# Optimization experiments

Measured on AMD Instinct MI355X. Metric: run time of the kernel, lower is better.

## Reference

```python
import jax, jax.numpy as jnp
import numpy as np
from jax import lax

CROP = 4
DATA_RANGE = 255.0
KSIZE = 11


def _box_filter(x):
    # x: [B,1,H,W]; 11x11 uniform kernel, padding 5 (SAME), single channel
    k = jnp.ones((1, 1, KSIZE, KSIZE), dtype=x.dtype) / (KSIZE * KSIZE)
    return lax.conv_general_dilated(
        x, k, window_strides=(1, 1), padding=[(5, 5), (5, 5)],
        dimension_numbers=("NCHW", "OIHW", "NCHW"))


def setup_inputs() -> dict:
    key = jax.random.key(0)
    k1, k2 = jax.random.split(key)
    img1 = jax.random.uniform(k1, (16, 3, 512, 512), dtype=jnp.float32) * DATA_RANGE
    img2 = jax.random.uniform(k2, (16, 3, 512, 512), dtype=jnp.float32) * DATA_RANGE
    return {"img1": img1, "img2": img2}


def reference(img1, img2):
    # only_test_y_channel: take channel 0
    x1 = img1[:, 0:1, :, :]
    x2 = img2[:, 0:1, :, :]
    # crop_border = 4
    x1 = x1[:, :, CROP:-CROP, CROP:-CROP].astype(jnp.float32)
    x2 = x2[:, :, CROP:-CROP, CROP:-CROP].astype(jnp.float32)

    C1 = (0.01 * DATA_RANGE) ** 2
    C2 = (0.03 * DATA_RANGE) ** 2

    mu1 = _box_filter(x1)
    mu2 = _box_filter(x2)
    mu1_sq = mu1 * mu1
    mu2_sq = mu2 * mu2
    mu1_mu2 = mu1 * mu2
    sigma1_sq = _box_filter(x1 * x1) - mu1_sq
    sigma2_sq = _box_filter(x2 * x2) - mu2_sq
    sigma12 = _box_filter(x1 * x2) - mu1_mu2

    ssim_map = ((2 * mu1_mu2 + C1) * (2 * sigma12 + C2)) / (
        (mu1_sq + mu2_sq + C1) * (sigma1_sq + sigma2_sq + C2))
    return jnp.mean(ssim_map)
```

## Files before the change

### kernel.cpp

```cpp
#include <hip/hip_runtime.h>

#define CROPPX 4
#define H 504
#define W 504
#define IMG 512
#define NB 16
#define NCH 3
#define KS 11
#define RAD 5
#define TW 64
#define STRIP (TW + 2*RAD)
#define RPS 18
#define NSEG 28
#define NXT 8
#define ROWS (RPS + 2*RAD)
#define CHUNK 7

__global__ __launch_bounds__(64) void ssim_main(const float* __restrict__ img1,
                                                const float* __restrict__ img2,
                                                float* __restrict__ partial) {
    const int tid = threadIdx.x;
    const int gx0 = blockIdx.x * TW;
    const int y0  = blockIdx.y * RPS;
    const int b   = blockIdx.z;

    __shared__ float2 strip[ROWS][STRIP];

    const float* p1 = img1 + (size_t)(b * NCH) * IMG * IMG + (size_t)CROPPX * IMG + CROPPX;
    const float* p2 = img2 + (size_t)(b * NCH) * IMG * IMG + (size_t)CROPPX * IMG + CROPPX;

    const int c0 = gx0 - RAD + tid;
    const int c1 = c0 + 64;
    const bool lane2 = tid < (STRIP - 64);
    const bool c0ok = (unsigned)c0 < (unsigned)W;
    const bool c1ok = lane2 && ((unsigned)c1 < (unsigned)W);

    #pragma unroll
    for (int rc = 0; rc < ROWS / CHUNK; ++rc) {
        float a0[CHUNK], b0[CHUNK], a1[CHUNK], b1[CHUNK];
        #pragma unroll
        for (int j = 0; j < CHUNK; ++j) {
            const int r = y0 - RAD + rc * CHUNK + j;
            a0[j] = 0.f; b0[j] = 0.f; a1[j] = 0.f; b1[j] = 0.f;
            if ((unsigned)r < (unsigned)H) {
                const size_t ro = (size_t)r * IMG;
                if (c0ok) { a0[j] = p1[ro + c0]; b0[j] = p2[ro + c0]; }
                if (c1ok) { a1[j] = p1[ro + c1]; b1[j] = p2[ro + c1]; }
            }
        }
        #pragma unroll
        for (int j = 0; j < CHUNK; ++j) {
            const int r = rc * CHUNK + j;
            strip[r][tid] = make_float2(a0[j], b0[j]);
            if (lane2) strip[r][64 + tid] = make_float2(a1[j], b1[j]);
        }
    }
    __syncthreads();

    float r1[KS], r2[KS], r11[KS], r22[KS], r12[KS];
    #pragma unroll
    for (int j = 0; j < KS; ++j) { r1[j]=0.f; r2[j]=0.f; r11[j]=0.f; r22[j]=0.f; r12[j]=0.f; }

    float vs1 = 0.f, vs2 = 0.f, vs11 = 0.f, vs22 = 0.f, vs12 = 0.f;
    float ssum = 0.f;
    const float C1 = 6.5025f, C2 = 58.5225f;
    const float inv121 = 1.0f / 121.0f;
    const bool colValid = (gx0 + tid) < W;

    for (int base = 0; base < ROWS; base += KS) {
        #pragma unroll
        for (int j = 0; j < KS; ++j) {
            const int iter = base + j;
            if (iter >= ROWS) break;

            float h1 = 0.f, h2 = 0.f, h11 = 0.f, h22 = 0.f, h12 = 0.f;
            #pragma unroll
            for (int dx = 0; dx < KS; ++dx) {
                const float2 ab = strip[iter][tid + dx];
                h1 += ab.x;
                h2 += ab.y;
                h11 = fmaf(ab.x, ab.x, h11);
                h22 = fmaf(ab.y, ab.y, h22);
                h12 = fmaf(ab.x, ab.y, h12);
            }

            vs1  += h1  - r1[j];  r1[j]  = h1;
            vs2  += h2  - r2[j];  r2[j]  = h2;
            vs11 += h11 - r11[j]; r11[j] = h11;
            vs22 += h22 - r22[j]; r22[j] = h22;
            vs12 += h12 - r12[j]; r12[j] = h12;

            if (iter >= 2 * RAD && colValid) {
                const float mu1 = vs1 * inv121;
                const float mu2 = vs2 * inv121;
                const float mu1s = mu1 * mu1;
                const float mu2s = mu2 * mu2;
                const float m12  = mu1 * mu2;
                const float s1  = fmaf(vs11, inv121, -mu1s);
                const float s2  = fmaf(vs22, inv121, -mu2s);
                const float s12 = fmaf(vs12, inv121, -m12);
                const float num = (2.0f * m12 + C1) * (2.0f * s12 + C2);
                const float den = (mu1s + mu2s + C1) * (s1 + s2 + C2);
                ssum = fmaf(num, __builtin_amdgcn_rcpf(den), ssum);
            }
        }
    }

    for (int off = 32; off > 0; off >>= 1)
        ssum += __shfl_down(ssum, off);
    if (tid == 0) {
        const int bidx = (blockIdx.z * gridDim.y + blockIdx.y) * gridDim.x + blockIdx.x;
        partial[bidx] = ssum;
    }
}

__global__ __launch_bounds__(256) void ssim_final(const float* __restrict__ partial,
                                                  int n, float* __restrict__ out) {
    __shared__ double sh[256];
    double s = 0.0;
    for (int i = threadIdx.x; i < n; i += 256) s += (double)partial[i];
    sh[threadIdx.x] = s;
    __syncthreads();
    for (int stride = 128; stride > 0; stride >>= 1) {
        if (threadIdx.x < stride) sh[threadIdx.x] += sh[threadIdx.x + stride];
        __syncthreads();
    }
    if (threadIdx.x == 0)
        out[0] = (float)(sh[0] / ((double)NB * (double)H * (double)W));
}

extern "C" void kernel_launch(void* const* d_in, const int* in_sizes, int n_in,
                              void* d_out, int out_size, void* d_ws, size_t ws_size,
                              hipStream_t stream) {
    const float* img1 = (const float*)d_in[0];
    const float* img2 = (const float*)d_in[1];
    float* out = (float*)d_out;
    float* partial = (float*)d_ws;

    dim3 grid(NXT, NSEG, NB);
    ssim_main<<<grid, 64, 0, stream>>>(img1, img2, partial);
    ssim_final<<<1, 256, 0, stream>>>(partial, NXT * NSEG * NB, out);
}
```

Measured before the change: 143.7 us.

## Stream rows through an 11-row LDS ring buffer with register prefetch

The kernel no longer stages the whole row strip in shared memory behind a block barrier. It keeps an 11-row ring buffer in LDS and prefetches input rows two ahead in registers, using a wave barrier in place of __syncthreads. This overlaps global loads with compute and cuts LDS use per block. Rows per segment also go from 18 to 21, which reduces the number of blocks and the redundant halo loads. The loop is now fully unrolled over 31 rows, which may raise register pressure and code size, and the clamped unconditional loads add a few instructions.

```diff
diff --git a/kernel.cpp b/kernel.cpp
--- a/kernel.cpp
+++ b/kernel.cpp
@@ -10,11 +10,10 @@
 #define RAD 5
 #define TW 64
 #define STRIP (TW + 2*RAD)
-#define RPS 18
-#define NSEG 28
+#define RPS 21
+#define NSEG 24
 #define NXT 8
-#define ROWS (RPS + 2*RAD)
-#define CHUNK 7
+#define TOTAL (RPS + 2*RAD)
 
 __global__ __launch_bounds__(64) void ssim_main(const float* __restrict__ img1,
                                                 const float* __restrict__ img2,
@@ -24,38 +23,18 @@
     const int y0  = blockIdx.y * RPS;
     const int b   = blockIdx.z;
 
-    __shared__ float2 strip[ROWS][STRIP];
+    __shared__ float2 buf[KS][STRIP];
 
     const float* p1 = img1 + (size_t)(b * NCH) * IMG * IMG + (size_t)CROPPX * IMG + CROPPX;
     const float* p2 = img2 + (size_t)(b * NCH) * IMG * IMG + (size_t)CROPPX * IMG + CROPPX;
 
-    const int c0 = gx0 - RAD + tid;
-    const int c1 = c0 + 64;
+    const int  c0   = gx0 - RAD + tid;
+    const int  c0c  = min(max(c0, 0), W - 1);
+    const bool c0ok = (unsigned)c0 < (unsigned)W;
+    const int  c1   = c0 + 64;
+    const int  c1c  = min(c1, W - 1);
+    const bool c1ok = (unsigned)c1 < (unsigned)W;
     const bool lane2 = tid < (STRIP - 64);
-    const bool c0ok = (unsigned)c0 < (unsigned)W;
-    const bool c1ok = lane2 && ((unsigned)c1 < (unsigned)W);
-
-    #pragma unroll
-    for (int rc = 0; rc < ROWS / CHUNK; ++rc) {
-        float a0[CHUNK], b0[CHUNK], a1[CHUNK], b1[CHUNK];
-        #pragma unroll
-        for (int j = 0; j < CHUNK; ++j) {
-            const int r = y0 - RAD + rc * CHUNK + j;
-            a0[j] = 0.f; b0[j] = 0.f; a1[j] = 0.f; b1[j] = 0.f;
-            if ((unsigned)r < (unsigned)H) {
-                const size_t ro = (size_t)r * IMG;
-                if (c0ok) { a0[j] = p1[ro + c0]; b0[j] = p2[ro + c0]; }
-                if (c1ok) { a1[j] = p1[ro + c1]; b1[j] = p2[ro + c1]; }
-            }
-        }
-        #pragma unroll
-        for (int j = 0; j < CHUNK; ++j) {
-            const int r = rc * CHUNK + j;
-            strip[r][tid] = make_float2(a0[j], b0[j]);
-            if (lane2) strip[r][64 + tid] = make_float2(a1[j], b1[j]);
-        }
-    }
-    __syncthreads();
 
     float r1[KS], r2[KS], r11[KS], r22[KS], r12[KS];
     #pragma unroll
@@ -67,44 +46,70 @@
     const float inv121 = 1.0f / 121.0f;
     const bool colValid = (gx0 + tid) < W;
 
-    for (int base = 0; base < ROWS; base += KS) {
+    float sa0[2], sb0[2], sa1[2], sb1[2];
+
+    #define LOAD_ROW(slot, rowIdx)                                            \
+    {                                                                         \
+        const int r_  = (rowIdx);                                             \
+        const int rc_ = min(max(r_, 0), H - 1);                               \
+        const bool rok_ = (unsigned)r_ < (unsigned)H;                         \
+        const size_t ro_ = (size_t)rc_ * IMG;                                 \
+        const float ta0_ = p1[ro_ + c0c], tb0_ = p2[ro_ + c0c];               \
+        sa0[slot] = (rok_ && c0ok) ? ta0_ : 0.f;                              \
+        sb0[slot] = (rok_ && c0ok) ? tb0_ : 0.f;                              \
+        float ta1_ = 0.f, tb1_ = 0.f;                                         \
+        if (lane2) { ta1_ = p1[ro_ + c1c]; tb1_ = p2[ro_ + c1c]; }            \
+        sa1[slot] = (rok_ && c1ok) ? ta1_ : 0.f;                              \
+        sb1[slot] = (rok_ && c1ok) ? tb1_ : 0.f;                              \
+    }
+
+    LOAD_ROW(0, y0 - RAD)
+    LOAD_ROW(1, y0 - RAD + 1)
+
+    #pragma unroll
+    for (int iter = 0; iter < TOTAL; ++iter) {
+        const int slot = iter % KS;
+        const int par  = iter & 1;
+
+        buf[slot][tid] = make_float2(sa0[par], sb0[par]);
+        if (lane2) buf[slot][64 + tid] = make_float2(sa1[par], sb1[par]);
+
+        if (iter + 2 < TOTAL) LOAD_ROW(par, y0 - RAD + iter + 2)
+
+        __builtin_amdgcn_wave_barrier();
+
+        float h1 = 0.f, h2 = 0.f, h11 = 0.f, h22 = 0.f, h12 = 0.f;
         #pragma unroll
-        for (int j = 0; j < KS; ++j) {
-            const int iter = base + j;
-            if (iter >= ROWS) break;
+        for (int dx = 0; dx < KS; ++dx) {
+            const float2 ab = buf[slot][tid + dx];
+            h1 += ab.x;
+            h2 += ab.y;
+            h11 = fmaf(ab.x, ab.x, h11);
+            h22 = fmaf(ab.y, ab.y, h22);
+            h12 = fmaf(ab.x, ab.y, h12);
+        }
 
-            float h1 = 0.f, h2 = 0.f, h11 = 0.f, h22 = 0.f, h12 = 0.f;
-            #pragma unroll
-            for (int dx = 0; dx < KS; ++dx) {
-                const float2 ab = strip[iter][tid + dx];
-                h1 += ab.x;
-                h2 += ab.y;
-                h11 = fmaf(ab.x, ab.x, h11);
-                h22 = fmaf(ab.y, ab.y, h22);
-                h12 = fmaf(ab.x, ab.y, h12);
-            }
+        vs1  += h1  - r1[slot];  r1[slot]  = h1;
+        vs2  += h2  - r2[slot];  r2[slot]  = h2;
+        vs11 += h11 - r11[slot]; r11[slot] = h11;
+        vs22 += h22 - r22[slot]; r22[slot] = h22;
+        vs12 += h12 - r12[slot]; r12[slot] = h12;
 
-            vs1  += h1  - r1[j];  r1[j]  = h1;
-            vs2  += h2  - r2[j];  r2[j]  = h2;
-            vs11 += h11 - r11[j]; r11[j] = h11;
-            vs22 += h22 - r22[j]; r22[j] = h22;
-            vs12 += h12 - r12[j]; r12[j] = h12;
-
-            if (iter >= 2 * RAD && colValid) {
-                const float mu1 = vs1 * inv121;
-                const float mu2 = vs2 * inv121;
-                const float mu1s = mu1 * mu1;
-                const float mu2s = mu2 * mu2;
-                const float m12  = mu1 * mu2;
-                const float s1  = fmaf(vs11, inv121, -mu1s);
-                const float s2  = fmaf(vs22, inv121, -mu2s);
-                const float s12 = fmaf(vs12, inv121, -m12);
-                const float num = (2.0f * m12 + C1) * (2.0f * s12 + C2);
-                const float den = (mu1s + mu2s + C1) * (s1 + s2 + C2);
-                ssum = fmaf(num, __builtin_amdgcn_rcpf(den), ssum);
-            }
+        if (iter >= 2 * RAD && colValid) {
+            const float mu1 = vs1 * inv121;
+            const float mu2 = vs2 * inv121;
+            const float mu1s = mu1 * mu1;
+            const float mu2s = mu2 * mu2;
+            const float m12  = mu1 * mu2;
+            const float s1  = fmaf(vs11, inv121, -mu1s);
+            const float s2  = fmaf(vs22, inv121, -mu2s);
+            const float s12 = fmaf(vs12, inv121, -m12);
+            const float num = (2.0f * m12 + C1) * (2.0f * s12 + C2);
+            const float den = (mu1s + mu2s + C1) * (s1 + s2 + C2);
+            ssum = fmaf(num, __builtin_amdgcn_rcpf(den), ssum);
         }
     }
+    #undef LOAD_ROW
 
     for (int off = 32; off > 0; off >>= 1)
         ssum += __shfl_down(ssum, off);
```

Result: faster. 135.6 us (-5.7%).
